# Performance work log

Hardware: AMD Instinct MI355X
Metric: run time of the kernel (lower is better)

The kernel has to match this reference:

```python
import jax, jax.numpy as jnp
import numpy as np

N_NODES = 100000
N_EDGES = 1600000
F_IN = 256
HID = 128
N_CLS = 64
K_APPNP = 10
ALPHA = 0.1


def setup_inputs() -> dict:
    key = jax.random.key(0)
    ks = jax.random.split(key, 12)
    x = jax.random.normal(ks[0], (N_NODES, F_IN), dtype=jnp.float32)
    edge_index = jax.random.randint(ks[1], (2, N_EDGES), 0, N_NODES, dtype=jnp.int64)
    def lin(k, fan_in, fan_out):
        s = 1.0 / np.sqrt(fan_in)
        kw, kb = jax.random.split(k)
        W = jax.random.uniform(kw, (fan_in, fan_out), minval=-s, maxval=s, dtype=jnp.float32)
        b = jax.random.uniform(kb, (fan_out,), minval=-s, maxval=s, dtype=jnp.float32)
        return W, b
    W1, b1 = lin(ks[2], F_IN, HID)
    W2, b2 = lin(ks[3], HID, HID)
    Wc, bc = lin(ks[4], HID, N_CLS)
    We, be = lin(ks[5], N_CLS, N_CLS)
    return {"x": x, "edge_index": edge_index, "W1": W1, "b1": b1, "W2": W2,
            "b2": b2, "Wc": Wc, "bc": bc, "We": We, "be": be}


def reference(x, edge_index, W1, b1, W2, b2, Wc, bc, We, be):
    N = x.shape[0]
    loop = jnp.arange(N)
    row = jnp.concatenate([edge_index[0], loop])  # source nodes (+ self loops)
    col = jnp.concatenate([edge_index[1], loop])  # target nodes (+ self loops)
    # symmetric GCN normalization: deg computed on targets
    deg = jax.ops.segment_sum(jnp.ones_like(col, dtype=x.dtype), col, num_segments=N)
    dinv = jnp.where(deg > 0, jax.lax.rsqrt(deg), 0.0)
    norm = dinv[row] * dinv[col]  # [E+N]

    def prop(h):  # normalized scatter-add aggregation
        return jax.ops.segment_sum(h[row] * norm[:, None], col, num_segments=N)

    # GCNConv: transform -> propagate -> bias (dropout is eval no-op)
    h = jax.nn.relu(prop(x @ W1) + b1)
    h = jax.nn.relu(prop(h @ W2) + b2)
    logits = h @ Wc + bc
    ev = jax.nn.relu(logits @ We + be)
    # APPNP: z_{k+1} = (1-alpha) * A_hat z_k + alpha * ev
    z = ev
    for _ in range(K_APPNP):
        z = (1.0 - ALPHA) * prop(z) + ALPHA * ev
    return jax.nn.log_softmax(z, axis=1)
```

## Files before the change

kernel.cpp:

```cpp
#include <hip/hip_runtime.h>
#include <hip/hip_fp16.h>


struct __align__(16) half8 { __half2 h[4]; };
typedef _Float16 f16x8 __attribute__((ext_vector_type(8)));
typedef float f32x4 __attribute__((ext_vector_type(4)));

__device__ __forceinline__ f16x8 cvt8(const float4& a, const float4& b) {
    f16x8 r;
    r[0] = (_Float16)a.x; r[1] = (_Float16)a.y; r[2] = (_Float16)a.z; r[3] = (_Float16)a.w;
    r[4] = (_Float16)b.x; r[5] = (_Float16)b.y; r[6] = (_Float16)b.z; r[7] = (_Float16)b.w;
    return r;
}

__global__ __launch_bounds__(256) void k_scanA(const int* __restrict__ deg, int* bs, int N) {
    __shared__ int s[256];
    int t = threadIdx.x;
    int i = blockIdx.x * 256 + t;
    int c = (i < N) ? deg[i] : 0;
    s[t] = c; __syncthreads();
    for (int o = 128; o > 0; o >>= 1) {
        if (t < o) s[t] += s[t + o];
        __syncthreads();
    }
    if (t == 0) bs[blockIdx.x] = s[0];
}

__global__ __launch_bounds__(512) void k_scanB(int* bs, int NB) {
    __shared__ int s[512];
    int t = threadIdx.x;
    int v = (t < NB) ? bs[t] : 0;
    s[t] = v; __syncthreads();
    for (int o = 1; o < 512; o <<= 1) {
        int u = (t >= o) ? s[t - o] : 0;
        __syncthreads();
        s[t] += u;
        __syncthreads();
    }
    if (t < NB) bs[t] = s[t] - v;
}

__global__ __launch_bounds__(256) void k_scanC(const int* __restrict__ deg, const int* __restrict__ bs,
                                               int* row_ptr, float* dinv, int N) {
    __shared__ int s[256];
    int t = threadIdx.x;
    int i = blockIdx.x * 256 + t;
    int c = (i < N) ? deg[i] : 0;
    s[t] = c; __syncthreads();
    for (int o = 1; o < 256; o <<= 1) {
        int u = (t >= o) ? s[t - o] : 0;
        __syncthreads();
        s[t] += u;
        __syncthreads();
    }
    if (i < N) {
        int off = bs[blockIdx.x];
        row_ptr[i] = off + s[t] - c;
        dinv[i] = rsqrtf((float)(deg[i] + 1));
        if (i == N - 1) row_ptr[N] = off + s[t];
    }
}

__global__ __launch_bounds__(256) void k_fill(const int* __restrict__ src, const int* __restrict__ dst,
                                              const int* __restrict__ row_ptr,
                                              const int* __restrict__ rank,
                                              int* __restrict__ csr_src, int E) {
    int e = blockIdx.x * 256 + threadIdx.x;
    if (e < E) csr_src[row_ptr[dst[e]] + rank[e]] = src[e];
}

__global__ __launch_bounds__(256) void k_prep(const float* __restrict__ W1,
                                              const float* __restrict__ W2,
                                              const float* __restrict__ Wc,
                                              const float* __restrict__ bc,
                                              const float* __restrict__ We,
                                              const float* __restrict__ be,
                                              __half* __restrict__ W1t,
                                              __half* __restrict__ W2t,
                                              __half* __restrict__ Wft,
                                              float* __restrict__ bf) {
    __shared__ float sWe[64 * 64];
    const int b = blockIdx.x, tid = threadIdx.x;
    if (b < 128) {
        int idx = b * 256 + tid;
        int j = idx & 7, n = (idx >> 3) & 127, qk = idx >> 10;
        int quad = qk & 3, kc = qk >> 2;
        int k = kc * 32 + quad * 8 + j;
        W1t[idx] = __float2half(W1[k * 128 + n]);
    } else if (b < 192) {
        int idx = (b - 128) * 256 + tid;
        int j = idx & 7, n = (idx >> 3) & 127, qk = idx >> 10;
        int quad = qk & 3, kc = qk >> 2;
        int k = kc * 32 + quad * 8 + j;
        W2t[idx] = __float2half(W2[k * 128 + n]);
    } else {
        for (int i = tid; i < 64 * 64 / 4; i += 256)
            ((float4*)sWe)[i] = ((const float4*)We)[i];
        __syncthreads();
        for (int idx = tid; idx < 128 * 64; idx += 256) {
            int r = idx >> 6, c = idx & 63;
            float s = 0.f;
#pragma unroll 8
            for (int j = 0; j < 64; j++) s += Wc[r * 64 + j] * sWe[j * 64 + c];
            int kc = r >> 5, quad = (r >> 3) & 3, jj = r & 7;
            Wft[(((kc * 4 + quad) * 64) + c) * 8 + jj] = __float2half(s);
        }
        if (tid < 64) {
            float s = be[tid];
#pragma unroll 8
            for (int j = 0; j < 64; j++) s += bc[j] * sWe[j * 64 + tid];
            bf[tid] = s;
        }
    }
}

template <int K, bool IN_F16, bool COUNT>
__global__ __launch_bounds__(512, 4) void k_gemm(const void* __restrict__ Xv,
                                                 const __half* __restrict__ Wtf,
                                                 const float* __restrict__ dinv,
                                                 __half* __restrict__ Y, int N,
                                                 const int* __restrict__ dst,
                                                 int* __restrict__ deg,
                                                 int* __restrict__ rank,
                                                 int E) {
    constexpr int NK = K / 32;
    constexpr int ITER = K / 32;
    __shared__ __align__(16) __half sB[K * 128];

    const int tid = threadIdx.x;

    int r4[4];
    int ebase = 0, estr = 0;
    if constexpr (COUNT) {
        ebase = blockIdx.x * 512 + tid;
        estr  = gridDim.x * 512;
        int d4[4];
#pragma unroll
        for (int i = 0; i < 4; ++i) {
            int e = ebase + i * estr;
            d4[i] = (e < E) ? dst[e] : 0;
        }
#pragma unroll
        for (int i = 0; i < 4; ++i) {
            int e = ebase + i * estr;
            r4[i] = (e < E) ? atomicAdd(&deg[d4[i]], 1) : 0;
        }
        for (int e = ebase + 4 * estr; e < E; e += estr)
            rank[e] = atomicAdd(&deg[dst[e]], 1);
    }

    const int wv = tid >> 6, ln = tid & 63;
    const int m = ln & 15, quad = ln >> 4;
    const int rowBase = blockIdx.x * 128 + wv * 16;
    int rowA = rowBase + m;
    if (rowA > N - 1) rowA = N - 1;

    const float*  xf = (const float*)Xv;
    const __half* xh = (const __half*)Xv;
    const long aOff = (long)rowA * K + quad * 8;

    f16x8 a8[4];
    float4 t0[4], t1[4];
    if constexpr (IN_F16) {
#pragma unroll
        for (int kc = 0; kc < NK; ++kc)
            a8[kc] = *(const f16x8*)&xh[aOff + kc * 32];
    } else {
#pragma unroll
        for (int c = 0; c < 4; ++c) {
            t0[c] = *(const float4*)&xf[aOff + c * 32];
            t1[c] = *(const float4*)&xf[aOff + c * 32 + 4];
        }
    }

    {
        f16x8 tb[ITER];
        const f16x8* g = (const f16x8*)Wtf;
#pragma unroll
        for (int i = 0; i < ITER; ++i) tb[i] = g[(i * 8 + wv) * 64 + ln];
        f16x8* l = (f16x8*)sB;
#pragma unroll
        for (int i = 0; i < ITER; ++i) l[(i * 8 + wv) * 64 + ln] = tb[i];
    }
    __syncthreads();

    if constexpr (!IN_F16) {
#pragma unroll
        for (int c = 0; c < 4; ++c) a8[c] = cvt8(t0[c], t1[c]);
#pragma unroll
        for (int c = 0; c < 4; ++c) {
            t0[c] = *(const float4*)&xf[aOff + (c + 4) * 32];
            t1[c] = *(const float4*)&xf[aOff + (c + 4) * 32 + 4];
        }
    }

    f32x4 d[8];
#pragma unroll
    for (int ct = 0; ct < 8; ++ct) d[ct] = {0.f, 0.f, 0.f, 0.f};

#pragma unroll
    for (int h = 0; h < NK / 4; ++h) {
        if constexpr (!IN_F16) {
            if (h == 1) {
#pragma unroll
                for (int c = 0; c < 4; ++c) a8[c] = cvt8(t0[c], t1[c]);
            }
        }
#pragma unroll
        for (int kq = 0; kq < 4; ++kq) {
            const int kc = h * 4 + kq;
            const f16x8 a = a8[IN_F16 ? kc : kq];
            const __half* bb = &sB[(size_t)(kc * 4 + quad) * 128 * 8];
#pragma unroll
            for (int ct = 0; ct < 8; ++ct) {
                const f16x8 b = *(const f16x8*)&bb[(ct * 16 + m) * 8];
                d[ct] = __builtin_amdgcn_mfma_f32_16x16x32_f16(a, b, d[ct], 0, 0, 0);
            }
        }
    }

#pragma unroll
    for (int ct = 0; ct < 8; ++ct) {
        const int col = ct * 16 + m;
#pragma unroll
        for (int reg = 0; reg < 4; ++reg) {
            const int row = rowBase + quad * 4 + reg;
            if (row < N) {
                if constexpr (COUNT)
                    Y[(long)row * 128 + col] = __float2half(d[ct][reg]);
                else
                    Y[(long)row * 128 + col] = __float2half(d[ct][reg] * dinv[row]);
            }
        }
    }

    if constexpr (COUNT) {
#pragma unroll
        for (int i = 0; i < 4; ++i) {
            int e = ebase + i * estr;
            if (e < E) rank[e] = r4[i];
        }
    }
}

__global__ __launch_bounds__(512, 4) void k_cls(const __half* __restrict__ H,
                                                const __half* __restrict__ Wtf,
                                                const float* __restrict__ bf,
                                                const float* __restrict__ dinv,
                                                float* __restrict__ ev,
                                                __half* __restrict__ evs, int N) {
    __shared__ __align__(16) __half sB[128 * 64];
    const int tid = threadIdx.x;
    const int wv = tid >> 6, ln = tid & 63;
    const int m = ln & 15, quad = ln >> 4;
    const int rowBase = blockIdx.x * 128 + wv * 16;
    int rowA = rowBase + m;
    if (rowA > N - 1) rowA = N - 1;
    const long aOff = (long)rowA * 128 + quad * 8;

    f16x8 a8[4];
#pragma unroll
    for (int kc = 0; kc < 4; ++kc)
        a8[kc] = *(const f16x8*)&H[aOff + kc * 32];

    {
        f16x8 tb[2];
        const f16x8* g = (const f16x8*)Wtf;
#pragma unroll
        for (int i = 0; i < 2; ++i) tb[i] = g[(i * 8 + wv) * 64 + ln];
        f16x8* l = (f16x8*)sB;
#pragma unroll
        for (int i = 0; i < 2; ++i) l[(i * 8 + wv) * 64 + ln] = tb[i];
    }
    __syncthreads();

    f32x4 d[4];
#pragma unroll
    for (int ct = 0; ct < 4; ++ct) d[ct] = {0.f, 0.f, 0.f, 0.f};

#pragma unroll
    for (int kc = 0; kc < 4; ++kc) {
        const __half* bb = &sB[(size_t)(kc * 4 + quad) * 64 * 8];
#pragma unroll
        for (int ct = 0; ct < 4; ++ct) {
            const f16x8 b = *(const f16x8*)&bb[(ct * 16 + m) * 8];
            d[ct] = __builtin_amdgcn_mfma_f32_16x16x32_f16(a8[kc], b, d[ct], 0, 0, 0);
        }
    }

#pragma unroll
    for (int ct = 0; ct < 4; ++ct) {
        const int col = ct * 16 + m;
#pragma unroll
        for (int reg = 0; reg < 4; ++reg) {
            const int row = rowBase + quad * 4 + reg;
            if (row < N) {
                float v = fmaxf(d[ct][reg] + bf[col], 0.f);
                ev[(long)row * 64 + col] = v;
                evs[(long)row * 64 + col] = __float2half(v * dinv[row]);
            }
        }
    }
}

template <int F, int MODE>
__global__ __launch_bounds__(256) void k_prop2(const __half* __restrict__ tab,
                                               const int* __restrict__ row_ptr,
                                               const int* __restrict__ csr_src,
                                               const float* __restrict__ dinv,
                                               const float* __restrict__ bias,
                                               const void* __restrict__ evx,
                                               void* __restrict__ out, int N) {
    constexpr int LPE = F / 8;
    constexpr int S = 64 / LPE;
    int wave = threadIdx.x >> 6;
    int lane = threadIdx.x & 63;
    int node = blockIdx.x * 4 + wave;
    if (node >= N) return;
    int slot = lane / LPE;
    int fl = lane % LPE;
    const int2 se = *(const int2*)&row_ptr[node];
    int s = se.x, e = se.y;

    float acc[8], accB[8];
#pragma unroll
    for (int q = 0; q < 8; q++) { acc[q] = 0.f; accB[q] = 0.f; }

    int j = s + slot;
    int i0 = 0, i1 = 0;
    if (j < e) i0 = csr_src[j];
    if (j + S < e) i1 = csr_src[j + S];
    while (j + S < e) {
        const int jn = j + 2 * S;
        int n0 = 0, n1 = 0;
        if (jn < e) n0 = csr_src[jn];
        if (jn + S < e) n1 = csr_src[jn + S];
        const half8 a = *(const half8*)&tab[(long)i0 * F + 8 * fl];
        const half8 b = *(const half8*)&tab[(long)i1 * F + 8 * fl];
        if (MODE == 4) {
            float da = dinv[i0], db = dinv[i1];
#pragma unroll
            for (int q = 0; q < 4; q++) {
                float2 fa = __half22float2(a.h[q]);
                float2 fb = __half22float2(b.h[q]);
                acc[2 * q] += da * fa.x; acc[2 * q + 1] += da * fa.y;
                accB[2 * q] += db * fb.x; accB[2 * q + 1] += db * fb.y;
            }
        } else {
#pragma unroll
            for (int q = 0; q < 4; q++) {
                float2 fa = __half22float2(a.h[q]);
                float2 fb = __half22float2(b.h[q]);
                acc[2 * q] += fa.x; acc[2 * q + 1] += fa.y;
                accB[2 * q] += fb.x; accB[2 * q + 1] += fb.y;
            }
        }
        i0 = n0; i1 = n1; j = jn;
    }
    if (j < e) {
        const half8 a = *(const half8*)&tab[(long)i0 * F + 8 * fl];
        if (MODE == 4) {
            float da = dinv[i0];
#pragma unroll
            for (int q = 0; q < 4; q++) {
                float2 fa = __half22float2(a.h[q]);
                acc[2 * q] += da * fa.x; acc[2 * q + 1] += da * fa.y;
            }
        } else {
#pragma unroll
            for (int q = 0; q < 4; q++) {
                float2 fa = __half22float2(a.h[q]);
                acc[2 * q] += fa.x; acc[2 * q + 1] += fa.y;
            }
        }
    }
    if (slot == 0) {
        const half8 a = *(const half8*)&tab[(long)node * F + 8 * fl];
        float ds = (MODE == 4) ? dinv[node] : 1.f;
#pragma unroll
        for (int q = 0; q < 4; q++) {
            float2 fa = __half22float2(a.h[q]);
            acc[2 * q] += ds * fa.x; acc[2 * q + 1] += ds * fa.y;
        }
    }
#pragma unroll
    for (int q = 0; q < 8; q++) acc[q] += accB[q];

#pragma unroll
    for (int off = LPE; off < 64; off <<= 1) {
#pragma unroll
        for (int q = 0; q < 8; q++) acc[q] += __shfl_xor(acc[q], off, 64);
    }

    if (slot == 0) {
        float di = dinv[node];
        if (MODE == 3 || MODE == 4) {
            const float4 b0 = *(const float4*)&bias[8 * fl];
            const float4 b1 = *(const float4*)&bias[8 * fl + 4];
            half8 ov;
            ov.h[0] = __floats2half2_rn(fmaxf(di * acc[0] + b0.x, 0.f),
                                        fmaxf(di * acc[1] + b0.y, 0.f));
            ov.h[1] = __floats2half2_rn(fmaxf(di * acc[2] + b0.z, 0.f),
                                        fmaxf(di * acc[3] + b0.w, 0.f));
            ov.h[2] = __floats2half2_rn(fmaxf(di * acc[4] + b1.x, 0.f),
                                        fmaxf(di * acc[5] + b1.y, 0.f));
            ov.h[3] = __floats2half2_rn(fmaxf(di * acc[6] + b1.z, 0.f),
                                        fmaxf(di * acc[7] + b1.w, 0.f));
            *(half8*)&((__half*)out)[(long)node * F + 8 * fl] = ov;
        } else if (MODE == 1) {
            float d2 = 0.9f * di * di;
            const half8 eh = *(const half8*)&((const __half*)evx)[(long)node * F + 8 * fl];
            half8 ov;
#pragma unroll
            for (int q = 0; q < 4; q++) {
                float2 ef = __half22float2(eh.h[q]);
                float vx = d2 * acc[2 * q] + 0.1f * ef.x;
                float vy = d2 * acc[2 * q + 1] + 0.1f * ef.y;
                ov.h[q] = __floats2half2_rn(vx, vy);
            }
            *(half8*)&((__half*)out)[(long)node * F + 8 * fl] = ov;
        } else {
            float d1 = 0.9f * di;
            const float* ef = (const float*)evx + (long)node * F + 8 * fl;
            const float4 e0 = *(const float4*)ef;
            const float4 e1 = *(const float4*)(ef + 4);
            float v[8];
            v[0] = d1 * acc[0] + 0.1f * e0.x;
            v[1] = d1 * acc[1] + 0.1f * e0.y;
            v[2] = d1 * acc[2] + 0.1f * e0.z;
            v[3] = d1 * acc[3] + 0.1f * e0.w;
            v[4] = d1 * acc[4] + 0.1f * e1.x;
            v[5] = d1 * acc[5] + 0.1f * e1.y;
            v[6] = d1 * acc[6] + 0.1f * e1.z;
            v[7] = d1 * acc[7] + 0.1f * e1.w;
            float m = v[0];
#pragma unroll
            for (int q = 1; q < 8; q++) m = fmaxf(m, v[q]);
#pragma unroll
            for (int off = 1; off < LPE; off <<= 1) m = fmaxf(m, __shfl_xor(m, off, 64));
            float ssum = 0.f;
#pragma unroll
            for (int q = 0; q < 8; q++) ssum += __expf(v[q] - m);
#pragma unroll
            for (int off = 1; off < LPE; off <<= 1) ssum += __shfl_xor(ssum, off, 64);
            float lse = m + __logf(ssum);
            float* o = (float*)out + (long)node * F + 8 * fl;
            float4 v0, v1;
            v0.x = v[0] - lse; v0.y = v[1] - lse; v0.z = v[2] - lse; v0.w = v[3] - lse;
            v1.x = v[4] - lse; v1.y = v[5] - lse; v1.z = v[6] - lse; v1.w = v[7] - lse;
            *(float4*)o = v0;
            *(float4*)(o + 4) = v1;
        }
    }
}

extern "C" void kernel_launch(void* const* d_in, const int* in_sizes, int n_in,
                              void* d_out, int out_size, void* d_ws, size_t ws_size,
                              hipStream_t stream) {
    const float* x  = (const float*)d_in[0];
    const int* edges = (const int*)d_in[1];
    const float* W1 = (const float*)d_in[2];
    const float* b1 = (const float*)d_in[3];
    const float* W2 = (const float*)d_in[4];
    const float* b2 = (const float*)d_in[5];
    const float* Wc = (const float*)d_in[6];
    const float* bc = (const float*)d_in[7];
    const float* We = (const float*)d_in[8];
    const float* be = (const float*)d_in[9];

    const int N = in_sizes[0] / 256;
    const int E = in_sizes[1] / 2;
    const int* esrc = edges;
    const int* edst = edges + E;

    char* ws = (char*)d_ws;
    size_t off = 0;
    auto alloc = [&](size_t bytes) -> void* {
        void* p = ws + off;
        off += (bytes + 255) & ~(size_t)255;
        return p;
    };
    int*    deg     = (int*)alloc((size_t)N * 4);
    int*    row_ptr = (int*)alloc((size_t)(N + 1) * 4);
    float*  dinv    = (float*)alloc((size_t)N * 4);
    int*    bs      = (int*)alloc(4096 * 4);
    int*    rank    = (int*)alloc((size_t)E * 4);
    int*    csr_src = (int*)alloc((size_t)E * 4);
    __half* P       = (__half*)alloc((size_t)N * 128 * 2);
    __half* Q16     = (__half*)alloc((size_t)N * 128 * 2);
    __half* zA      = (__half*)alloc((size_t)N * 64 * 2);
    __half* zB      = (__half*)alloc((size_t)N * 64 * 2);
    __half* evs     = (__half*)alloc((size_t)N * 64 * 2);
    float*  bf      = (float*)alloc(64 * 4);
    __half* W1t     = (__half*)alloc(128 * 256 * 2);
    __half* W2t     = (__half*)alloc(128 * 128 * 2);
    __half* Wft     = (__half*)alloc(64 * 128 * 2);
    float*  ev      = (float*)d_out;

    const int nbN = (N + 255) / 256;
    const int nbE = (E + 255) / 256;
    const int nbP = (N + 3) / 4;
    const int TG  = (N + 127) / 128;

    hipMemsetAsync(deg, 0, (size_t)N * 4, stream);
    k_prep<<<193, 256, 0, stream>>>(W1, W2, Wc, bc, We, be, W1t, W2t, Wft, bf);
    k_gemm<256, false, true><<<TG, 512, 0, stream>>>(x, W1t, nullptr, P, N,
                                                     edst, deg, rank, E);

    k_scanA<<<nbN, 256, 0, stream>>>(deg, bs, N);
    k_scanB<<<1, 512, 0, stream>>>(bs, nbN);
    k_scanC<<<nbN, 256, 0, stream>>>(deg, bs, row_ptr, dinv, N);
    k_fill<<<nbE, 256, 0, stream>>>(esrc, edst, row_ptr, rank, csr_src, E);

    k_prop2<128, 4><<<nbP, 256, 0, stream>>>(P, row_ptr, csr_src, dinv, b1, nullptr, Q16, N);

    k_gemm<128, true, false><<<TG, 512, 0, stream>>>(Q16, W2t, dinv, P, N,
                                                     nullptr, nullptr, nullptr, 0);
    k_prop2<128, 3><<<nbP, 256, 0, stream>>>(P, row_ptr, csr_src, dinv, b2, nullptr, Q16, N);

    k_cls<<<TG, 512, 0, stream>>>(Q16, Wft, bf, dinv, ev, evs, N);

    const __half* zin = evs;
    __half* zout;
    for (int it = 0; it < 9; ++it) {
        zout = (it % 2 == 0) ? zA : zB;
        k_prop2<64, 1><<<nbP, 256, 0, stream>>>(zin, row_ptr, csr_src, dinv, nullptr, evs, zout, N);
        zin = zout;
    }
    k_prop2<64, 2><<<nbP, 256, 0, stream>>>(zin, row_ptr, csr_src, dinv, nullptr, ev, (float*)d_out, N);
}
```

Baseline: 941.5 us.

## Split propagation kernels into feature chunks across the grid

Makes the aggregation kernel handle a 16-feature column slice per block, with the grid scaled by the number of chunks (8 for 128 features, 4 for 64 features). The final log-softmax pass keeps full width. Each chunk gathers one 32-byte half8 segment per neighbor, so each wave covers many more edges in parallel, and consecutive launches work on narrower column bands that may sit better in cache. The cost is that CSR indices and dinv are re-read once per chunk and each gathered row segment is only 32 bytes, which may waste memory transactions.

```diff
diff --git a/kernel.cpp b/kernel.cpp
--- a/kernel.cpp
+++ b/kernel.cpp
@@ -303,19 +303,22 @@
     }
 }
 
-template <int F, int MODE>
+template <int F, int FC, int MODE>
 __global__ __launch_bounds__(256) void k_prop2(const __half* __restrict__ tab,
                                                const int* __restrict__ row_ptr,
                                                const int* __restrict__ csr_src,
                                                const float* __restrict__ dinv,
                                                const float* __restrict__ bias,
                                                const void* __restrict__ evx,
-                                               void* __restrict__ out, int N) {
-    constexpr int LPE = F / 8;
+                                               void* __restrict__ out, int N, int nbP) {
+    constexpr int LPE = FC / 8;
     constexpr int S = 64 / LPE;
     int wave = threadIdx.x >> 6;
     int lane = threadIdx.x & 63;
-    int node = blockIdx.x * 4 + wave;
+    const int chunk = blockIdx.x / nbP;
+    const int nb = blockIdx.x - chunk * nbP;
+    const int fo = chunk * FC;
+    int node = nb * 4 + wave;
     if (node >= N) return;
     int slot = lane / LPE;
     int fl = lane % LPE;
@@ -335,8 +338,8 @@
         int n0 = 0, n1 = 0;
         if (jn < e) n0 = csr_src[jn];
         if (jn + S < e) n1 = csr_src[jn + S];
-        const half8 a = *(const half8*)&tab[(long)i0 * F + 8 * fl];
-        const half8 b = *(const half8*)&tab[(long)i1 * F + 8 * fl];
+        const half8 a = *(const half8*)&tab[(long)i0 * F + fo + 8 * fl];
+        const half8 b = *(const half8*)&tab[(long)i1 * F + fo + 8 * fl];
         if (MODE == 4) {
             float da = dinv[i0], db = dinv[i1];
 #pragma unroll
@@ -358,7 +361,7 @@
         i0 = n0; i1 = n1; j = jn;
     }
     if (j < e) {
-        const half8 a = *(const half8*)&tab[(long)i0 * F + 8 * fl];
+        const half8 a = *(const half8*)&tab[(long)i0 * F + fo + 8 * fl];
         if (MODE == 4) {
             float da = dinv[i0];
 #pragma unroll
@@ -375,7 +378,7 @@
         }
     }
     if (slot == 0) {
-        const half8 a = *(const half8*)&tab[(long)node * F + 8 * fl];
+        const half8 a = *(const half8*)&tab[(long)node * F + fo + 8 * fl];
         float ds = (MODE == 4) ? dinv[node] : 1.f;
 #pragma unroll
         for (int q = 0; q < 4; q++) {
@@ -395,8 +398,8 @@
     if (slot == 0) {
         float di = dinv[node];
         if (MODE == 3 || MODE == 4) {
-            const float4 b0 = *(const float4*)&bias[8 * fl];
-            const float4 b1 = *(const float4*)&bias[8 * fl + 4];
+            const float4 b0 = *(const float4*)&bias[fo + 8 * fl];
+            const float4 b1 = *(const float4*)&bias[fo + 8 * fl + 4];
             half8 ov;
             ov.h[0] = __floats2half2_rn(fmaxf(di * acc[0] + b0.x, 0.f),
                                         fmaxf(di * acc[1] + b0.y, 0.f));
@@ -406,10 +409,10 @@
                                         fmaxf(di * acc[5] + b1.y, 0.f));
             ov.h[3] = __floats2half2_rn(fmaxf(di * acc[6] + b1.z, 0.f),
                                         fmaxf(di * acc[7] + b1.w, 0.f));
-            *(half8*)&((__half*)out)[(long)node * F + 8 * fl] = ov;
+            *(half8*)&((__half*)out)[(long)node * F + fo + 8 * fl] = ov;
         } else if (MODE == 1) {
             float d2 = 0.9f * di * di;
-            const half8 eh = *(const half8*)&((const __half*)evx)[(long)node * F + 8 * fl];
+            const half8 eh = *(const half8*)&((const __half*)evx)[(long)node * F + fo + 8 * fl];
             half8 ov;
 #pragma unroll
             for (int q = 0; q < 4; q++) {
@@ -418,7 +421,7 @@
                 float vy = d2 * acc[2 * q + 1] + 0.1f * ef.y;
                 ov.h[q] = __floats2half2_rn(vx, vy);
             }
-            *(half8*)&((__half*)out)[(long)node * F + 8 * fl] = ov;
+            *(half8*)&((__half*)out)[(long)node * F + fo + 8 * fl] = ov;
         } else {
             float d1 = 0.9f * di;
             const float* ef = (const float*)evx + (long)node * F + 8 * fl;
@@ -512,11 +515,11 @@
     k_scanC<<<nbN, 256, 0, stream>>>(deg, bs, row_ptr, dinv, N);
     k_fill<<<nbE, 256, 0, stream>>>(esrc, edst, row_ptr, rank, csr_src, E);
 
-    k_prop2<128, 4><<<nbP, 256, 0, stream>>>(P, row_ptr, csr_src, dinv, b1, nullptr, Q16, N);
+    k_prop2<128, 16, 4><<<8 * nbP, 256, 0, stream>>>(P, row_ptr, csr_src, dinv, b1, nullptr, Q16, N, nbP);
 
     k_gemm<128, true, false><<<TG, 512, 0, stream>>>(Q16, W2t, dinv, P, N,
                                                      nullptr, nullptr, nullptr, 0);
-    k_prop2<128, 3><<<nbP, 256, 0, stream>>>(P, row_ptr, csr_src, dinv, b2, nullptr, Q16, N);
+    k_prop2<128, 16, 3><<<8 * nbP, 256, 0, stream>>>(P, row_ptr, csr_src, dinv, b2, nullptr, Q16, N, nbP);
 
     k_cls<<<TG, 512, 0, stream>>>(Q16, Wft, bf, dinv, ev, evs, N);
 
@@ -524,8 +527,8 @@
     __half* zout;
     for (int it = 0; it < 9; ++it) {
         zout = (it % 2 == 0) ? zA : zB;
-        k_prop2<64, 1><<<nbP, 256, 0, stream>>>(zin, row_ptr, csr_src, dinv, nullptr, evs, zout, N);
+        k_prop2<64, 16, 1><<<4 * nbP, 256, 0, stream>>>(zin, row_ptr, csr_src, dinv, nullptr, evs, zout, N, nbP);
         zin = zout;
     }
-    k_prop2<64, 2><<<nbP, 256, 0, stream>>>(zin, row_ptr, csr_src, dinv, nullptr, ev, (float*)d_out, N);
-}
+    k_prop2<64, 64, 2><<<nbP, 256, 0, stream>>>(zin, row_ptr, csr_src, dinv, nullptr, ev, (float*)d_out, N, nbP);
+}
```

New measurement: 2.553 ms. +171.2%, slower.
